# Optimization experiments

Hardware: AMD Instinct MI355X
Metric: run time of the kernel (lower is better)

## Reference

```python
import jax, jax.numpy as jnp
import numpy as np
from jax.scipy.special import logsumexp

# Complete binary tree, heap indexing: node i has children 2i+1, 2i+2.
# Edge for child c (c >= 1) is edge_pot[c-1], shape [C, C]:
#   rows = parent state, cols = child state (matches torch code's
#   logsumexp(edge + msg, dim=1) upward and edge.T downward).
DEPTH = 18
C = 16
N = 2 ** (DEPTH + 1) - 1  # 524287 nodes, N-1 edges


def setup_inputs() -> dict:
    key = jax.random.key(0)
    k1, k2 = jax.random.split(key)
    unary = jax.random.normal(k1, (N, C), dtype=jnp.float32)
    edge_pot = jax.random.normal(k2, (N - 1, C, C), dtype=jnp.float32)
    return {"unary": unary, "edge_pot": edge_pot, "depth": DEPTH}


def reference(unary, edge_pot, depth):
    """Sum-product belief propagation on a complete binary tree.

    Returns beliefs [N, C]: for each node v,
      belief[v] = unary[v] + sum(up messages from children) + down message from parent,
    identical to the per-message torch BFS loop, but processed level-parallel.
    """
    c = unary.shape[1]
    # ---------- upward pass (leaves -> root) ----------
    # subtotal[v] = unary[v] + sum of up-messages from v's children (V2F to parent factor)
    subtotal = unary
    m_up = jnp.zeros_like(unary)  # m_up[ch] = F2V message from edge (parent, ch) to parent
    for d in range(depth, 0, -1):
        lo, hi = 2 ** d - 1, 2 ** (d + 1) - 1          # children level, size 2^d
        ep = edge_pot[lo - 1:hi - 1]                    # [2^d, C, C]
        # logsumexp over child state (axis 2): torch's logsumexp(edge + msg, dim=1)
        msg = logsumexp(ep + subtotal[lo:hi][:, None, :], axis=2)  # [2^d, C]
        m_up = m_up.at[lo:hi].set(msg)
        plo, phi = 2 ** (d - 1) - 1, 2 ** d - 1
        # children of consecutive parents are consecutive pairs (2p+1, 2p+2)
        subtotal = subtotal.at[plo:phi].add(msg.reshape(-1, 2, c).sum(axis=1))
    # ---------- downward pass (root -> leaves) ----------
    m_down = jnp.zeros_like(unary)  # m_down[ch] = F2V message from edge (parent, ch) to ch
    for d in range(1, depth + 1):
        lo, hi = 2 ** d - 1, 2 ** (d + 1) - 1
        plo, phi = 2 ** (d - 1) - 1, 2 ** d - 1
        # V2F from parent p towards child ch: all incoming F2V at p except m_up[ch]
        par_total = jnp.repeat(subtotal[plo:phi] + m_down[plo:phi], 2, axis=0)  # [2^d, C]
        v2f = par_total - m_up[lo:hi]
        ep_t = jnp.swapaxes(edge_pot[lo - 1:hi - 1], 1, 2)  # edge.T: [2^d, Cchild, Cparent]
        msg = logsumexp(ep_t + v2f[:, None, :], axis=2)     # logsumexp over parent state
        m_down = m_down.at[lo:hi].set(msg)
    return subtotal + m_down  # beliefs [N, C]
```

## Files before the change

kernel.cpp:

```cpp
#include <hip/hip_runtime.h>
#include <stdint.h>


#define EPC 256

__device__ __forceinline__ void ldvec16(const float* p, float* d) {
    const float4* q = (const float4*)p;
    #pragma unroll
    for (int t = 0; t < 4; ++t) {
        float4 a = q[t];
        d[4*t+0] = a.x; d[4*t+1] = a.y; d[4*t+2] = a.z; d[4*t+3] = a.w;
    }
}

__device__ __forceinline__ float lse16_rs(const float* r, const float* s) {
    float v[16];
    float m;
    #pragma unroll
    for (int j = 0; j < 16; ++j) {
        v[j] = r[j] + s[j];
        m = (j == 0) ? v[0] : fmaxf(m, v[j]);
    }
    float acc = 0.f;
    #pragma unroll
    for (int j = 0; j < 16; ++j) acc += __expf(v[j] - m);
    return m + __logf(acc);
}

__device__ __forceinline__ void enc_row(uint8_t* dst, const float* E) {
    int w[4];
    #pragma unroll
    for (int t = 0; t < 4; ++t) {
        int x = __builtin_amdgcn_cvt_pk_fp8_f32(E[4*t+0], E[4*t+1], 0, false);
        x     = __builtin_amdgcn_cvt_pk_fp8_f32(E[4*t+2], E[4*t+3], x, true);
        w[t] = x;
    }
    *(int4*)dst = make_int4(w[0], w[1], w[2], w[3]);
}

__device__ __forceinline__ void dec_row(const uint8_t* src, float* E) {
    uint4 w = *(const uint4*)src;
    uint32_t a;
    a = w.x;
    E[0]  = __builtin_amdgcn_cvt_f32_fp8(a, 0);
    E[1]  = __builtin_amdgcn_cvt_f32_fp8(a, 1);
    E[2]  = __builtin_amdgcn_cvt_f32_fp8(a, 2);
    E[3]  = __builtin_amdgcn_cvt_f32_fp8(a, 3);
    a = w.y;
    E[4]  = __builtin_amdgcn_cvt_f32_fp8(a, 0);
    E[5]  = __builtin_amdgcn_cvt_f32_fp8(a, 1);
    E[6]  = __builtin_amdgcn_cvt_f32_fp8(a, 2);
    E[7]  = __builtin_amdgcn_cvt_f32_fp8(a, 3);
    a = w.z;
    E[8]  = __builtin_amdgcn_cvt_f32_fp8(a, 0);
    E[9]  = __builtin_amdgcn_cvt_f32_fp8(a, 1);
    E[10] = __builtin_amdgcn_cvt_f32_fp8(a, 2);
    E[11] = __builtin_amdgcn_cvt_f32_fp8(a, 3);
    a = w.w;
    E[12] = __builtin_amdgcn_cvt_f32_fp8(a, 0);
    E[13] = __builtin_amdgcn_cvt_f32_fp8(a, 1);
    E[14] = __builtin_amdgcn_cvt_f32_fp8(a, 2);
    E[15] = __builtin_amdgcn_cvt_f32_fp8(a, 3);
}

__device__ __forceinline__ uint16_t f32_to_bf16(float x) {
    uint32_t u = __float_as_uint(x);
    u += 0x7fff + ((u >> 16) & 1);
    return (uint16_t)(u >> 16);
}
__device__ __forceinline__ float bf16_to_f32(uint16_t h) {
    return __uint_as_float((uint32_t)h << 16);
}

template <bool USE8>
__global__ __launch_bounds__(256) void up_flat(
    const float* __restrict__ csrc, const float* __restrict__ unary,
    const float* __restrict__ ep, float* __restrict__ out,
    uint8_t* __restrict__ e8, uint16_t* __restrict__ mup,
    int plo, int pcount) {
    int t = blockIdx.x * 256 + threadIdx.x;
    if (t >= pcount * 16) return;
    int i = t & 15;
    size_t p = (size_t)plo + (t >> 4);
    size_t cl = 2 * p + 1;

    float msg[2];
    #pragma unroll
    for (int ch = 0; ch < 2; ++ch) {
        size_t c = cl + ch;
        float s[16], r[16];
        ldvec16(csrc + c * 16, s);
        ldvec16(ep + (c - 1) * 256 + i * 16, r);
        if (USE8) {
            float E[16];
            #pragma unroll
            for (int j = 0; j < 16; ++j) E[j] = __expf(r[j]);
            enc_row(e8 + (c - 1) * EPC + i * 16, E);
            float m = s[0];
            #pragma unroll
            for (int j = 1; j < 16; ++j) m = fmaxf(m, s[j]);
            float acc = 0.f;
            #pragma unroll
            for (int j = 0; j < 16; ++j) acc += E[j] * __expf(s[j] - m);
            msg[ch] = __logf(acc) + m;
            mup[c * 16 + i] = f32_to_bf16(msg[ch]);
        } else {
            msg[ch] = lse16_rs(r, s);
        }
    }
    out[p * 16 + i] = unary[p * 16 + i] + msg[0] + msg[1];
}

template <bool USE8>
__global__ __launch_bounds__(256) void down_flat(
    const float* __restrict__ ssrc, const float* __restrict__ ep,
    const uint8_t* __restrict__ e8, const uint16_t* __restrict__ mup,
    float* __restrict__ out, int lo, int count) {
    if (!USE8) {
        int t = blockIdx.x * 256 + threadIdx.x;
        if (t >= count * 16) return;
        int i = t & 15;
        size_t v = (size_t)lo + (t >> 4);
        size_t par = (v - 1) >> 1;
        float s[16], r[16];
        ldvec16(ssrc + v * 16, s);
        float sub_i = ssrc[v * 16 + i];
        ldvec16(ep + (v - 1) * 256 + i * 16, r);
        float mu = lse16_rs(r, s);
        float v2f = out[par * 16 + i] - mu;
        const float* nb = ep + (v - 1) * 256 + i;
        float c[16];
        #pragma unroll
        for (int k = 0; k < 16; ++k) c[k] = nb[k * 16];
        float vv[16], m;
        #pragma unroll
        for (int k = 0; k < 16; ++k) {
            float x = c[k] + __shfl(v2f, k, 16);
            vv[k] = x;
            m = (k == 0) ? x : fmaxf(m, x);
        }
        float acc = 0.f;
        #pragma unroll
        for (int k = 0; k < 16; ++k) acc += __expf(vv[k] - m);
        out[v * 16 + i] = sub_i + m + __logf(acc);
        return;
    }
    __shared__ float T[16][16][20];
    int g = threadIdx.x >> 4, i = threadIdx.x & 15;
    size_t v = (size_t)lo + (size_t)(blockIdx.x * 16 + g);
    size_t par = (v - 1) >> 1;

    float sub_i = ssrc[v * 16 + i];
    float pt    = out[par * 16 + i];
    float mu    = bf16_to_f32(mup[v * 16 + i]);
    float v2f   = pt - mu;

    float m = v2f;
    m = fmaxf(m, __shfl_xor(m, 1, 16));
    m = fmaxf(m, __shfl_xor(m, 2, 16));
    m = fmaxf(m, __shfl_xor(m, 4, 16));
    m = fmaxf(m, __shfl_xor(m, 8, 16));
    float u = __expf(v2f - m);

    float E[16];
    dec_row(e8 + (v - 1) * EPC + i * 16, E);
    #pragma unroll
    for (int j = 0; j < 16; ++j) T[g][i][j] = E[j] * u;
    __syncthreads();
    float acc = 0.f;
    #pragma unroll
    for (int k = 0; k < 16; ++k) acc += T[g][k][i];

    out[v * 16 + i] = sub_i + __logf(acc) + m;
}

__global__ __launch_bounds__(256) void up_sub_f32(
    const float* __restrict__ unary, const float* __restrict__ ep,
    float* __restrict__ out, int rl, int dl, int depth) {
    __shared__ float sub[2][32][16];
    int j = blockIdx.x;
    int cur = 0;
    for (int d = dl; d > rl; --d) {
        int np = 1 << (d - 1 - rl);
        size_t pbase = (((size_t)1 << (d - 1)) - 1) + (size_t)j * np;
        bool fromGlobal = (d == dl);
        const float* gsrc = (d == depth) ? unary : out;
        for (int t = threadIdx.x; t < np * 16; t += 256) {
            int pl = t >> 4, i = t & 15;
            size_t p = pbase + pl;
            size_t cl = 2 * p + 1, cr = cl + 1;
            float s[16], r[16];

            if (fromGlobal) ldvec16(gsrc + cl * 16, s);
            else            ldvec16(&sub[cur ^ 1][2 * pl][0], s);
            ldvec16(ep + (cl - 1) * 256 + i * 16, r);
            float msgL = lse16_rs(r, s);

            if (fromGlobal) ldvec16(gsrc + cr * 16, s);
            else            ldvec16(&sub[cur ^ 1][2 * pl + 1][0], s);
            ldvec16(ep + (cr - 1) * 256 + i * 16, r);
            float msgR = lse16_rs(r, s);

            float v = unary[p * 16 + i] + msgL + msgR;
            out[p * 16 + i] = v;
            if (d - 1 > rl) sub[cur][pl][i] = v;
        }
        __syncthreads();
        cur ^= 1;
    }
}

__global__ __launch_bounds__(256) void down_sub_f32(
    const float* __restrict__ unary, const float* __restrict__ ep,
    float* __restrict__ out, int rl, int dl, int depth) {
    __shared__ float bel[2][32][16];
    int j = blockIdx.x;
    int cur = 0;
    for (int d = rl + 1; d <= dl; ++d) {
        int nc = 1 << (d - rl);
        size_t cbase = (((size_t)1 << d) - 1) + (size_t)j * nc;
        bool leaf = (d == depth);
        bool parGlobal = (d == rl + 1);
        for (int t = threadIdx.x; t < nc * 16; t += 256) {
            int vl = t >> 4, i = t & 15;
            size_t v = cbase + vl;
            const float* ssrc = leaf ? unary : out;
            float s[16], r[16];
            ldvec16(ssrc + v * 16, s);
            float sub_i = ssrc[v * 16 + i];
            ldvec16(ep + (v - 1) * 256 + i * 16, r);
            float mu = lse16_rs(r, s);

            float pt;
            if (parGlobal) pt = out[((v - 1) >> 1) * 16 + i];
            else           pt = bel[cur ^ 1][vl >> 1][i];
            float v2f = pt - mu;

            const float* nb = ep + (v - 1) * 256 + i;
            float c[16];
            #pragma unroll
            for (int k = 0; k < 16; ++k) c[k] = nb[k * 16];

            float vv[16], m;
            #pragma unroll
            for (int k = 0; k < 16; ++k) {
                float x = c[k] + __shfl(v2f, k, 16);
                vv[k] = x;
                m = (k == 0) ? x : fmaxf(m, x);
            }
            float acc = 0.f;
            #pragma unroll
            for (int k = 0; k < 16; ++k) acc += __expf(vv[k] - m);
            float b = sub_i + m + __logf(acc);
            out[v * 16 + i] = b;
            if (d < dl) bel[cur][vl][i] = b;
        }
        __syncthreads();
        cur ^= 1;
    }
}

__device__ __forceinline__ void up_body_f32(const float* __restrict__ unary,
                                            const float* __restrict__ ep,
                                            float* out, size_t p, int i) {
    size_t cl = 2 * p + 1, cr = cl + 1;
    float s[16], r[16];
    ldvec16(out + cl * 16, s);
    ldvec16(ep + (cl - 1) * 256 + i * 16, r);
    float msgL = lse16_rs(r, s);
    ldvec16(out + cr * 16, s);
    ldvec16(ep + (cr - 1) * 256 + i * 16, r);
    float msgR = lse16_rs(r, s);
    out[p * 16 + i] = unary[p * 16 + i] + msgL + msgR;
}

__device__ __forceinline__ void down_body_f32(const float* __restrict__ ep,
                                              float* out, size_t v, int i) {
    size_t par = (v - 1) >> 1;
    float s[16], r[16];
    ldvec16(out + v * 16, s);
    float sub_i = out[v * 16 + i];
    ldvec16(ep + (v - 1) * 256 + i * 16, r);
    float mu = lse16_rs(r, s);
    float v2f = out[par * 16 + i] - mu;
    const float* nb = ep + (v - 1) * 256 + i;
    float c[16];
    #pragma unroll
    for (int k = 0; k < 16; ++k) c[k] = nb[k * 16];
    float vv[16], m;
    #pragma unroll
    for (int k = 0; k < 16; ++k) {
        float x = c[k] + __shfl(v2f, k, 16);
        vv[k] = x;
        m = (k == 0) ? x : fmaxf(m, x);
    }
    float acc = 0.f;
    #pragma unroll
    for (int k = 0; k < 16; ++k) acc += __expf(vv[k] - m);
    out[v * 16 + i] = sub_i + m + __logf(acc);
}

__global__ __launch_bounds__(1024) void top_fused(const float* __restrict__ unary,
                                                  const float* __restrict__ ep,
                                                  float* out, int FD) {
    int tid = threadIdx.x;
    for (int d = FD; d >= 1; --d) {
        int pcount = 1 << (d - 1);
        size_t plo = pcount - 1;
        for (int t = tid; t < pcount * 16; t += blockDim.x)
            up_body_f32(unary, ep, out, plo + (t >> 4), t & 15);
        __syncthreads();
    }
    for (int d = 1; d <= FD; ++d) {
        int count = 1 << d;
        size_t lo = count - 1;
        for (int t = tid; t < count * 16; t += blockDim.x)
            down_body_f32(ep, out, lo + (t >> 4), t & 15);
        __syncthreads();
    }
}

extern "C" void kernel_launch(void* const* d_in, const int* in_sizes, int n_in,
                              void* d_out, int out_size, void* d_ws, size_t ws_size,
                              hipStream_t stream) {
    const float* unary = (const float*)d_in[0];
    const float* ep    = (const float*)d_in[1];
    float* out = (float*)d_out;

    int Nn = in_sizes[0] / 16;
    int depth = 0;
    while ((1 << (depth + 1)) < Nn + 1) ++depth;

    uint8_t* e8 = (uint8_t*)d_ws;
    size_t e8_bytes = (size_t)Nn * EPC;
    size_t mup_off = (e8_bytes + 255) & ~(size_t)255;
    uint16_t* mup = (uint16_t*)((uint8_t*)d_ws + mup_off);
    size_t need = mup_off + (size_t)Nn * 16 * 2;
    bool use8 = ws_size >= need;

    if (use8 && depth >= 13) {
        for (int d = depth; d >= 13; --d) {
            int pcount = 1 << (d - 1);
            int plo = pcount - 1;
            const float* csrc = (d == depth) ? unary : out;
            up_flat<true><<<pcount * 16 / 256, 256, 0, stream>>>(
                csrc, unary, ep, out, e8, mup, plo, pcount);
        }
        up_sub_f32<<<64, 256, 0, stream>>>(unary, ep, out, 6, 12, depth);
        top_fused<<<1, 1024, 0, stream>>>(unary, ep, out, 6);
        down_sub_f32<<<64, 256, 0, stream>>>(unary, ep, out, 6, 12, depth);
        for (int d = 13; d <= depth; ++d) {
            int count = 1 << d;
            int lo = count - 1;
            const float* ssrc = (d == depth) ? unary : out;
            down_flat<true><<<count * 16 / 256, 256, 0, stream>>>(
                ssrc, ep, e8, mup, out, lo, count);
        }
    } else {
        int FD = (depth >= 2) ? ((depth - 1 < 6) ? depth - 1 : 6) : 0;
        for (int d = depth; d > FD; --d) {
            int pcount = 1 << (d - 1);
            int plo = pcount - 1;
            const float* csrc = (d == depth) ? unary : out;
            dim3 grid((pcount * 16 + 255) / 256);
            up_flat<false><<<grid, 256, 0, stream>>>(
                csrc, unary, ep, out, e8, mup, plo, pcount);
        }
        if (FD > 0)
            top_fused<<<1, 1024, 0, stream>>>(unary, ep, out, FD);
        for (int d = FD + 1; d <= depth; ++d) {
            int count = 1 << d;
            int lo = count - 1;
            const float* ssrc = (d == depth) ? unary : out;
            dim3 grid((count * 16 + 255) / 256);
            down_flat<false><<<grid, 256, 0, stream>>>(
                ssrc, ep, e8, mup, out, lo, count);
        }
    }
}
```

Measured before the change: 249.9 us.

## Replace sub-tree kernels with flat per-level launches down to level 7 and fused top6 kernel

Removes the 64-block up_sub_f32/down_sub_f32 kernels that handled levels 7-12 and instead runs the per-level up_flat/down_flat fp8 kernels down to level 7. The top six levels are now handled by a new single-block top6 kernel that keeps fp8-encoded exponentiated edge potentials, up messages and subtotals in shared memory. The aim is to replace the poorly parallel 64-block sub-tree kernels with fully parallel flat launches. In exchange it adds about a dozen extra small kernel launches and uses fp8 precision for the middle levels.

Result: no change. 252.8 us (+1.2%).

```diff
diff --git a/kernel.cpp b/kernel.cpp
--- a/kernel.cpp
+++ b/kernel.cpp
@@ -61,6 +61,10 @@
     E[13] = __builtin_amdgcn_cvt_f32_fp8(a, 1);
     E[14] = __builtin_amdgcn_cvt_f32_fp8(a, 2);
     E[15] = __builtin_amdgcn_cvt_f32_fp8(a, 3);
+}
+
+__device__ __forceinline__ float dec1(uint8_t b) {
+    return __builtin_amdgcn_cvt_f32_fp8((uint32_t)b, 0);
 }
 
 __device__ __forceinline__ uint16_t f32_to_bf16(float x) {
@@ -174,90 +178,83 @@
     out[v * 16 + i] = sub_i + __logf(acc) + m;
 }
 
-__global__ __launch_bounds__(256) void up_sub_f32(
-    const float* __restrict__ unary, const float* __restrict__ ep,
-    float* __restrict__ out, int rl, int dl, int depth) {
-    __shared__ float sub[2][32][16];
-    int j = blockIdx.x;
-    int cur = 0;
-    for (int d = dl; d > rl; --d) {
-        int np = 1 << (d - 1 - rl);
-        size_t pbase = (((size_t)1 << (d - 1)) - 1) + (size_t)j * np;
-        bool fromGlobal = (d == dl);
-        const float* gsrc = (d == depth) ? unary : out;
-        for (int t = threadIdx.x; t < np * 16; t += 256) {
-            int pl = t >> 4, i = t & 15;
-            size_t p = pbase + pl;
-            size_t cl = 2 * p + 1, cr = cl + 1;
-            float s[16], r[16];
-
-            if (fromGlobal) ldvec16(gsrc + cl * 16, s);
-            else            ldvec16(&sub[cur ^ 1][2 * pl][0], s);
-            ldvec16(ep + (cl - 1) * 256 + i * 16, r);
-            float msgL = lse16_rs(r, s);
-
-            if (fromGlobal) ldvec16(gsrc + cr * 16, s);
-            else            ldvec16(&sub[cur ^ 1][2 * pl + 1][0], s);
-            ldvec16(ep + (cr - 1) * 256 + i * 16, r);
-            float msgR = lse16_rs(r, s);
-
-            float v = unary[p * 16 + i] + msgL + msgR;
-            out[p * 16 + i] = v;
-            if (d - 1 > rl) sub[cur][pl][i] = v;
+__global__ __launch_bounds__(1024) void top6(const float* __restrict__ unary,
+                                             const float* __restrict__ ep,
+                                             float* __restrict__ out) {
+    __shared__ uint8_t epl[126 * 256];
+    __shared__ float sb[127][16];
+    __shared__ float mu[127][16];
+    __shared__ float un[63][16];
+    int tid = threadIdx.x;
+
+    for (int row = tid; row < 126 * 16; row += 1024) {
+        float r[16], E[16];
+        ldvec16(ep + (size_t)row * 16, r);
+        #pragma unroll
+        for (int j = 0; j < 16; ++j) E[j] = __expf(r[j]);
+        enc_row(&epl[row * 16], E);
+    }
+    {
+        int g = tid >> 4, i = tid & 15;
+        sb[63 + g][i] = out[(size_t)(63 + g) * 16 + i];
+    }
+    if (tid < 63 * 16) un[tid >> 4][tid & 15] = unary[tid];
+    __syncthreads();
+
+    #pragma unroll
+    for (int d = 6; d >= 1; --d) {
+        int pcount = 1 << (d - 1);
+        if (tid < pcount * 16) {
+            int pl = tid >> 4, i = tid & 15;
+            int p = pcount - 1 + pl;
+            float msg[2];
+            #pragma unroll
+            for (int ch = 0; ch < 2; ++ch) {
+                int c = 2 * p + 1 + ch;
+                float E[16], s[16];
+                dec_row(&epl[(c - 1) * 256 + i * 16], E);
+                ldvec16(&sb[c][0], s);
+                float m = s[0];
+                #pragma unroll
+                for (int j = 1; j < 16; ++j) m = fmaxf(m, s[j]);
+                float acc = 0.f;
+                #pragma unroll
+                for (int j = 0; j < 16; ++j) acc += E[j] * __expf(s[j] - m);
+                msg[ch] = __logf(acc) + m;
+                mu[c][i] = msg[ch];
+            }
+            sb[p][i] = un[p][i] + msg[0] + msg[1];
         }
         __syncthreads();
-        cur ^= 1;
-    }
-}
-
-__global__ __launch_bounds__(256) void down_sub_f32(
-    const float* __restrict__ unary, const float* __restrict__ ep,
-    float* __restrict__ out, int rl, int dl, int depth) {
-    __shared__ float bel[2][32][16];
-    int j = blockIdx.x;
-    int cur = 0;
-    for (int d = rl + 1; d <= dl; ++d) {
-        int nc = 1 << (d - rl);
-        size_t cbase = (((size_t)1 << d) - 1) + (size_t)j * nc;
-        bool leaf = (d == depth);
-        bool parGlobal = (d == rl + 1);
-        for (int t = threadIdx.x; t < nc * 16; t += 256) {
-            int vl = t >> 4, i = t & 15;
-            size_t v = cbase + vl;
-            const float* ssrc = leaf ? unary : out;
-            float s[16], r[16];
-            ldvec16(ssrc + v * 16, s);
-            float sub_i = ssrc[v * 16 + i];
-            ldvec16(ep + (v - 1) * 256 + i * 16, r);
-            float mu = lse16_rs(r, s);
-
-            float pt;
-            if (parGlobal) pt = out[((v - 1) >> 1) * 16 + i];
-            else           pt = bel[cur ^ 1][vl >> 1][i];
-            float v2f = pt - mu;
-
-            const float* nb = ep + (v - 1) * 256 + i;
-            float c[16];
-            #pragma unroll
-            for (int k = 0; k < 16; ++k) c[k] = nb[k * 16];
-
-            float vv[16], m;
-            #pragma unroll
-            for (int k = 0; k < 16; ++k) {
-                float x = c[k] + __shfl(v2f, k, 16);
-                vv[k] = x;
-                m = (k == 0) ? x : fmaxf(m, x);
-            }
+    }
+
+    #pragma unroll
+    for (int d = 1; d <= 6; ++d) {
+        int count = 1 << d;
+        if (tid < count * 16) {
+            int vl = tid >> 4, i = tid & 15;
+            int v = count - 1 + vl;
+            int par = (v - 1) >> 1;
+            float v2f = sb[par][i] - mu[v][i];
+            float m = v2f;
+            m = fmaxf(m, __shfl_xor(m, 1, 16));
+            m = fmaxf(m, __shfl_xor(m, 2, 16));
+            m = fmaxf(m, __shfl_xor(m, 4, 16));
+            m = fmaxf(m, __shfl_xor(m, 8, 16));
+            float u = __expf(v2f - m);
+            const uint8_t* nb = &epl[(v - 1) * 256];
             float acc = 0.f;
             #pragma unroll
-            for (int k = 0; k < 16; ++k) acc += __expf(vv[k] - m);
-            float b = sub_i + m + __logf(acc);
-            out[v * 16 + i] = b;
-            if (d < dl) bel[cur][vl][i] = b;
+            for (int k = 0; k < 16; ++k)
+                acc += dec1(nb[k * 16 + i]) * __shfl(u, k, 16);
+            float bel = sb[v][i] + __logf(acc) + m;
+            sb[v][i] = bel;
         }
         __syncthreads();
-        cur ^= 1;
-    }
+    }
+
+    const float* sbf = &sb[0][0];
+    for (int t = tid; t < 127 * 16; t += 1024) out[t] = sbf[t];
 }
 
 __device__ __forceinline__ void up_body_f32(const float* __restrict__ unary,
@@ -339,22 +336,18 @@
     bool use8 = ws_size >= need;
 
     if (use8 && depth >= 13) {
-        for (int d = depth; d >= 13; --d) {
+        for (int d = depth; d >= 7; --d) {
             int pcount = 1 << (d - 1);
-            int plo = pcount - 1;
             const float* csrc = (d == depth) ? unary : out;
             up_flat<true><<<pcount * 16 / 256, 256, 0, stream>>>(
-                csrc, unary, ep, out, e8, mup, plo, pcount);
-        }
-        up_sub_f32<<<64, 256, 0, stream>>>(unary, ep, out, 6, 12, depth);
-        top_fused<<<1, 1024, 0, stream>>>(unary, ep, out, 6);
-        down_sub_f32<<<64, 256, 0, stream>>>(unary, ep, out, 6, 12, depth);
-        for (int d = 13; d <= depth; ++d) {
+                csrc, unary, ep, out, e8, mup, pcount - 1, pcount);
+        }
+        top6<<<1, 1024, 0, stream>>>(unary, ep, out);
+        for (int d = 7; d <= depth; ++d) {
             int count = 1 << d;
-            int lo = count - 1;
             const float* ssrc = (d == depth) ? unary : out;
             down_flat<true><<<count * 16 / 256, 256, 0, stream>>>(
-                ssrc, ep, e8, mup, out, lo, count);
+                ssrc, ep, e8, mup, out, count - 1, count);
         }
     } else {
         int FD = (depth >= 2) ? ((depth - 1 < 6) ? depth - 1 : 6) : 0;
```
